# Kernel tuning notes

Hardware: AMD Instinct MI355X
Metric: run time of the kernel (lower is better)

The kernel has to match this reference:

```python
import jax, jax.numpy as jnp
import numpy as np

KERNEL_MUL = 2.0
KERNEL_NUM = 5


def setup_inputs() -> dict:
    key = jax.random.key(0)
    k1, k2 = jax.random.split(key)
    source = jax.random.normal(k1, (4096, 256), dtype=jnp.float32)
    target = jax.random.normal(k2, (4096, 256), dtype=jnp.float32)
    return {"source": source, "target": target}


def reference(source, target):
    n = source.shape[0]
    m = target.shape[0]
    total = jnp.concatenate([source, target], axis=0)  # [n+m, d]
    N = n + m
    # pairwise squared L2 distances via GEMM identity (same math as expand-based)
    sq = jnp.sum(total * total, axis=1)  # [N]
    d2 = sq[:, None] + sq[None, :] - 2.0 * (total @ total.T)  # [N, N]
    d2 = jnp.maximum(d2, 0.0)
    # bandwidth from detached distances (torch uses L2_distance.data)
    bandwidth = jax.lax.stop_gradient(jnp.sum(d2)) / (N * N - N)
    bandwidth = bandwidth / (KERNEL_MUL ** (KERNEL_NUM // 2))
    kernels = jnp.zeros_like(d2)
    for i in range(KERNEL_NUM):  # fixed small loop over bandwidths
        kernels = kernels + jnp.exp(-d2 / (bandwidth * (KERNEL_MUL ** i)))
    XX = jnp.mean(kernels[:n, :n])
    YY = jnp.mean(kernels[n:, n:])
    XY = jnp.mean(kernels[:n, n:])
    YX = jnp.mean(kernels[n:, :n])
    return XX + YY - XY - YX
```

## Files before the change

kernel.cpp:

```cpp
#include <hip/hip_runtime.h>
#include <hip/hip_bf16.h>
#include <stdint.h>
#include <math.h>

#define D     256
#define NTOT  8192
#define NSRC  4096
#define NT    64
#define NTRI  (NT * (NT + 1) / 2)
#define PREPB 256

using f32x4 = __attribute__((ext_vector_type(4))) float;

#define GLB_AS __attribute__((address_space(1)))
#define LDS_AS __attribute__((address_space(3)))

#if __has_builtin(__builtin_amdgcn_exp2f)
#define EXP2F __builtin_amdgcn_exp2f
#else
#define EXP2F exp2f
#endif

__device__ inline unsigned char f32_to_e4m3(float v) {
  uint32_t u = __float_as_uint(v);
  uint32_t s = (u >> 24) & 0x80u;
  uint32_t m = u & 0x7FFFFFFFu;
  if (m <= 0x3C000000u) return (unsigned char)s;
  if (m <  0x3C800000u) return (unsigned char)(s | 0x08u);
  if (m >= 0x43F00000u) return (unsigned char)(s | 0x7Eu);
  uint32_t r = m + 0x0007FFFFu + ((m >> 20) & 1u);
  uint32_t e = (r >> 23) - 127u + 7u;
  return (unsigned char)(s | (e << 3) | ((r >> 20) & 7u));
}
__device__ inline float e4m3_to_f32(unsigned char q) {
  uint32_t s = ((uint32_t)(q & 0x80u)) << 24;
  uint32_t em = q & 0x7Fu;
  if (em == 0) return __uint_as_float(s);
  uint32_t e = (em >> 3) + 120u;
  return __uint_as_float(s | (e << 23) | ((em & 7u) << 20));
}

#define OFF_XB   ((size_t)0)
#define OFF_SQ   ((size_t)NTOT * D)
#define OFF_CP   (OFF_SQ + (size_t)NTOT * 4)
#define OFF_SP   (OFF_CP + (size_t)PREPB * 256 * 4)
#define OFF_CF   (OFF_SP + (size_t)PREPB * 4)
#define OFF_PT   (OFF_CF + 32)
#define OFF_END  (OFF_PT + (size_t)NTRI * 4)

__global__ __launch_bounds__(256) void prep_kernel(
    const float* __restrict__ src, const float* __restrict__ tgt,
    unsigned char* __restrict__ xb, float* __restrict__ sq,
    float* __restrict__ colpart, float* __restrict__ sqpart)
{
  __shared__ float scol4[4][256];
  __shared__ float sSl[4];
  const int tid = threadIdx.x, wave = tid >> 6, lane = tid & 63;
  const int row0 = blockIdx.x * 32 + wave * 8;
  const float* p0 = (row0 < NSRC) ? (src + (size_t)row0 * D)
                                  : (tgt + (size_t)(row0 - NSRC) * D);
  float c0 = 0.f, c1 = 0.f, c2 = 0.f, c3 = 0.f, swave = 0.f;
  for (int rr = 0; rr < 8; ++rr) {
    const int row = row0 + rr;
    const float4 v = reinterpret_cast<const float4*>(p0 + (size_t)rr * D)[lane];
    uchar4 h;
    h.x = f32_to_e4m3(v.x); h.y = f32_to_e4m3(v.y);
    h.z = f32_to_e4m3(v.z); h.w = f32_to_e4m3(v.w);
    reinterpret_cast<uchar4*>(xb + (size_t)row * D)[lane] = h;
    const float f0 = e4m3_to_f32(h.x), f1 = e4m3_to_f32(h.y),
                f2 = e4m3_to_f32(h.z), f3 = e4m3_to_f32(h.w);
    c0 += f0; c1 += f1; c2 += f2; c3 += f3;
    float s = f0 * f0 + f1 * f1 + f2 * f2 + f3 * f3;
    #pragma unroll
    for (int off = 32; off > 0; off >>= 1) s += __shfl_down(s, off);
    if (lane == 0) { sq[row] = s; swave += s; }
  }
  scol4[wave][lane * 4 + 0] = c0;
  scol4[wave][lane * 4 + 1] = c1;
  scol4[wave][lane * 4 + 2] = c2;
  scol4[wave][lane * 4 + 3] = c3;
  if (lane == 0) sSl[wave] = swave;
  __syncthreads();
  colpart[blockIdx.x * 256 + tid] =
      scol4[0][tid] + scol4[1][tid] + scol4[2][tid] + scol4[3][tid];
  if (tid == 0) sqpart[blockIdx.x] = sSl[0] + sSl[1] + sSl[2] + sSl[3];
}

__global__ __launch_bounds__(256) void bw_kernel(
    const float* __restrict__ colpart, const float* __restrict__ sqpart,
    float* __restrict__ cf)
{
  __shared__ float red[256];
  const int t = threadIdx.x;
  float cs = 0.f;
  for (int b = 0; b < PREPB; ++b) cs += colpart[b * 256 + t];
  red[t] = cs * cs;
  __syncthreads();
  for (int off = 128; off > 0; off >>= 1) {
    if (t < off) red[t] += red[t + off];
    __syncthreads();
  }
  const float s2 = red[0];
  __syncthreads();
  red[t] = (t < PREPB) ? sqpart[t] : 0.f;
  __syncthreads();
  for (int off = 128; off > 0; off >>= 1) {
    if (t < off) red[t] += red[t + off];
    __syncthreads();
  }
  if (t == 0) {
    const double sumd2 = 2.0 * (double)NTOT * (double)red[0] - 2.0 * (double)s2;
    const double bw = sumd2 / ((double)NTOT * (double)NTOT - (double)NTOT) / 4.0;
    cf[0] = (float)(-1.4426950408889634 / (bw * 16.0));
  }
}

__global__ __launch_bounds__(256) void pair_kernel(
    const unsigned char* __restrict__ xb, const float* __restrict__ sq,
    const float* __restrict__ cf, float* __restrict__ part)
{
  const int idx = (blockIdx.x & 7) * (NTRI / 8) + (blockIdx.x >> 3);
  const float rr = sqrtf(4160.25f - 2.0f * (float)idx);
  int bi = (int)(64.5f - rr);
  while (NT * (bi + 1) - (bi + 1) * bi / 2 <= idx) ++bi;
  while (NT * bi - bi * (bi - 1) / 2 > idx) --bi;
  const int bj = bi + (idx - (NT * bi - bi * (bi - 1) / 2));

  __shared__ __align__(16) unsigned char lA[128 * 128];
  __shared__ __align__(16) unsigned char lB[128 * 128];
  __shared__ float sqA[128], sqB[128], wsum[4];

  const int tid = threadIdx.x, wave = tid >> 6, lane = tid & 63;
  const int wr = wave >> 1, wc = wave & 1;

  const float c4 = cf[0];
  if (tid < 128) sqA[tid] = sq[bi * 128 + tid];
  else           sqB[tid - 128] = sq[bj * 128 + (tid - 128)];

  const unsigned char* gA0 =
      xb + (size_t)(bi * 128 + wave * 32 + (lane >> 3)) * D + ((lane & 7) ^ (lane >> 3)) * 16;
  const unsigned char* gB0 =
      xb + (size_t)(bj * 128 + wave * 32 + (lane >> 3)) * D + ((lane & 7) ^ (lane >> 3)) * 16;
  char* dA = (char*)lA + wave * 4096;
  char* dB = (char*)lB + wave * 4096;

#define STAGE(t) do {                                                        \
    _Pragma("unroll")                                                        \
    for (int q = 0; q < 4; ++q) {                                            \
      __builtin_amdgcn_global_load_lds(                                      \
          (const GLB_AS uint32_t*)(gA0 + (size_t)q * 8 * D + (t) * 128),     \
          (LDS_AS uint32_t*)(dA + q * 1024), 16, 0, 0);                      \
      __builtin_amdgcn_global_load_lds(                                      \
          (const GLB_AS uint32_t*)(gB0 + (size_t)q * 8 * D + (t) * 128),     \
          (LDS_AS uint32_t*)(dB + q * 1024), 16, 0, 0);                      \
    } } while (0)

  f32x4 acc[4][4];
  #pragma unroll
  for (int mi = 0; mi < 4; ++mi)
    #pragma unroll
    for (int nj = 0; nj < 4; ++nj)
      acc[mi][nj] = (f32x4){0.f, 0.f, 0.f, 0.f};

  const int g = lane >> 4, r7 = lane & 7, rlow = lane & 15;
  const int off8 = (g & 1) * 8, ghalf = g >> 1;

  #pragma unroll
  for (int t = 0; t < 2; ++t) {
    STAGE(t);
    __syncthreads();
    #pragma unroll
    for (int ks = 0; ks < 4; ++ks) {
      const int slot = (2 * ks + ghalf);
      long af[4], bf[4];
      #pragma unroll
      for (int mi = 0; mi < 4; ++mi) {
        const int rowA = wr * 64 + mi * 16 + rlow;
        af[mi] = *(const long*)((const char*)lA + rowA * 128 +
                                (((slot ^ r7)) << 4) + off8);
      }
      #pragma unroll
      for (int nj = 0; nj < 4; ++nj) {
        const int rowB = wc * 64 + nj * 16 + rlow;
        bf[nj] = *(const long*)((const char*)lB + rowB * 128 +
                                (((slot ^ r7)) << 4) + off8);
      }
      #pragma unroll
      for (int mi = 0; mi < 4; ++mi)
        #pragma unroll
        for (int nj = 0; nj < 4; ++nj)
          acc[mi][nj] = __builtin_amdgcn_mfma_f32_16x16x32_fp8_fp8(
              af[mi], bf[nj], acc[mi][nj], 0, 0, 0);
    }
    if (t == 0) __syncthreads();
  }
#undef STAGE

  const int r0c = (lane >> 4) * 4, cc = lane & 15;
  float sjv[4];
  #pragma unroll
  for (int nj = 0; nj < 4; ++nj) sjv[nj] = sqB[wc * 64 + nj * 16 + cc];
  float tsum = 0.f;
  #pragma unroll
  for (int mi = 0; mi < 4; ++mi) {
    #pragma unroll
    for (int r = 0; r < 4; ++r) {
      const float si = sqA[wr * 64 + mi * 16 + r0c + r];
      #pragma unroll
      for (int nj = 0; nj < 4; ++nj) {
        float d2 = fmaf(-2.f, acc[mi][nj][r], si + sjv[nj]);
        d2 = fmaxf(d2, 0.f);
        const float e4 = EXP2F(d2 * c4);
        const float e3 = e4 * e4, e2 = e3 * e3;
        const float e1 = e2 * e2, e0 = e1 * e1;
        tsum += ((e4 + e3) + (e2 + e1)) + e0;
      }
    }
  }
  #pragma unroll
  for (int off = 32; off > 0; off >>= 1) tsum += __shfl_down(tsum, off);
  if (lane == 0) wsum[wave] = tsum;
  __syncthreads();
  if (tid == 0) part[idx] = wsum[0] + wsum[1] + wsum[2] + wsum[3];
}

__global__ __launch_bounds__(256) void out_kernel(
    const float* __restrict__ part, float* __restrict__ out)
{
  __shared__ double red0[256], red1[256], red2[256];
  const int t = threadIdx.x;
  double a0 = 0.0, a1 = 0.0, a2 = 0.0;
  for (int j = t; j < NTRI; j += 256) {
    const float r1 = sqrtf(4160.25f - 2.0f * (float)j);
    int bi = (int)(64.5f - r1);
    while (NT * (bi + 1) - (bi + 1) * bi / 2 <= j) ++bi;
    while (NT * bi - bi * (bi - 1) / 2 > j) --bi;
    const int bj = bi + (j - (NT * bi - bi * (bi - 1) / 2));
    const double w = (bi == bj) ? 1.0 : 2.0;
    const double v = w * (double)part[j];
    if (bi >= 32) a1 += v;
    else if (bj >= 32) a2 += v;
    else a0 += v;
  }
  red0[t] = a0; red1[t] = a1; red2[t] = a2;
  __syncthreads();
  for (int off = 128; off > 0; off >>= 1) {
    if (t < off) {
      red0[t] += red0[t + off];
      red1[t] += red1[t + off];
      red2[t] += red2[t + off];
    }
    __syncthreads();
  }
  if (t == 0)
    out[0] = (float)((red0[0] + red1[0] - red2[0]) /
                     ((double)NSRC * (double)NSRC));
}

extern "C" void kernel_launch(void* const* d_in, const int* in_sizes, int n_in,
                              void* d_out, int out_size, void* d_ws, size_t ws_size,
                              hipStream_t stream) {
  (void)in_sizes; (void)n_in; (void)out_size; (void)ws_size;
  const float* src = (const float*)d_in[0];
  const float* tgt = (const float*)d_in[1];
  char* ws = (char*)d_ws;
  unsigned char* xb = (unsigned char*)(ws + OFF_XB);
  float* sq      = (float*)(ws + OFF_SQ);
  float* colpart = (float*)(ws + OFF_CP);
  float* sqpart  = (float*)(ws + OFF_SP);
  float* cf      = (float*)(ws + OFF_CF);
  float* part    = (float*)(ws + OFF_PT);

  prep_kernel<<<PREPB, 256, 0, stream>>>(src, tgt, xb, sq, colpart, sqpart);
  bw_kernel<<<1, 256, 0, stream>>>(colpart, sqpart, cf);
  pair_kernel<<<NTRI, 256, 0, stream>>>(xb, sq, cf, part);
  out_kernel<<<1, 256, 0, stream>>>(part, (float*)d_out);
}
```

Before: 52.35 us.

## Double-buffer fp8 K-tiles in LDS with async prefetch and widen final reduction

Splits the K dimension of the pair kernel into four 64-byte chunks held in two ping-pong LDS buffers. The next chunk is prefetched with global_load_lds while MFMAs run on the current one, using explicit vmcnt waits, raw s_barrier calls and setprio around the MFMA block. The aim is to hide global-load latency that the old stage-then-sync loop exposed. The final reduction kernel also moves from 256 to 1024 threads. The cost is more barriers per tile and a new XOR swizzle for the narrower rows that must stay correct.

```diff
diff --git a/kernel.cpp b/kernel.cpp
--- a/kernel.cpp
+++ b/kernel.cpp
@@ -126,8 +126,8 @@
   while (NT * bi - bi * (bi - 1) / 2 > idx) --bi;
   const int bj = bi + (idx - (NT * bi - bi * (bi - 1) / 2));
 
-  __shared__ __align__(16) unsigned char lA[128 * 128];
-  __shared__ __align__(16) unsigned char lB[128 * 128];
+  __shared__ __align__(16) unsigned char lA[2][128 * 64];
+  __shared__ __align__(16) unsigned char lB[2][128 * 64];
   __shared__ float sqA[128], sqB[128], wsum[4];
 
   const int tid = threadIdx.x, wave = tid >> 6, lane = tid & 63;
@@ -138,21 +138,23 @@
   else           sqB[tid - 128] = sq[bj * 128 + (tid - 128)];
 
   const unsigned char* gA0 =
-      xb + (size_t)(bi * 128 + wave * 32 + (lane >> 3)) * D + ((lane & 7) ^ (lane >> 3)) * 16;
+      xb + (size_t)(bi * 128 + wave * 32 + (lane >> 2)) * D
+         + (((lane & 3) ^ ((lane >> 2) & 3)) * 16);
   const unsigned char* gB0 =
-      xb + (size_t)(bj * 128 + wave * 32 + (lane >> 3)) * D + ((lane & 7) ^ (lane >> 3)) * 16;
-  char* dA = (char*)lA + wave * 4096;
-  char* dB = (char*)lB + wave * 4096;
-
-#define STAGE(t) do {                                                        \
+      xb + (size_t)(bj * 128 + wave * 32 + (lane >> 2)) * D
+         + (((lane & 3) ^ ((lane >> 2) & 3)) * 16);
+
+#define STAGE(buf, t) do {                                                   \
+    char* dA_ = (char*)lA[buf] + wave * 2048;                                \
+    char* dB_ = (char*)lB[buf] + wave * 2048;                                \
     _Pragma("unroll")                                                        \
-    for (int q = 0; q < 4; ++q) {                                            \
+    for (int q = 0; q < 2; ++q) {                                            \
       __builtin_amdgcn_global_load_lds(                                      \
-          (const GLB_AS uint32_t*)(gA0 + (size_t)q * 8 * D + (t) * 128),     \
-          (LDS_AS uint32_t*)(dA + q * 1024), 16, 0, 0);                      \
+          (const GLB_AS uint32_t*)(gA0 + (size_t)q * 16 * D + (t) * 64),     \
+          (LDS_AS uint32_t*)(dA_ + q * 1024), 16, 0, 0);                     \
       __builtin_amdgcn_global_load_lds(                                      \
-          (const GLB_AS uint32_t*)(gB0 + (size_t)q * 8 * D + (t) * 128),     \
-          (LDS_AS uint32_t*)(dB + q * 1024), 16, 0, 0);                      \
+          (const GLB_AS uint32_t*)(gB0 + (size_t)q * 16 * D + (t) * 64),     \
+          (LDS_AS uint32_t*)(dB_ + q * 1024), 16, 0, 0);                     \
     } } while (0)
 
   f32x4 acc[4][4];
@@ -162,37 +164,50 @@
     for (int nj = 0; nj < 4; ++nj)
       acc[mi][nj] = (f32x4){0.f, 0.f, 0.f, 0.f};
 
-  const int g = lane >> 4, r7 = lane & 7, rlow = lane & 15;
+  const int g = lane >> 4, rlow = lane & 15, r3 = lane & 3;
   const int off8 = (g & 1) * 8, ghalf = g >> 1;
 
-  #pragma unroll
-  for (int t = 0; t < 2; ++t) {
-    STAGE(t);
-    __syncthreads();
-    #pragma unroll
-    for (int ks = 0; ks < 4; ++ks) {
-      const int slot = (2 * ks + ghalf);
+  STAGE(0, 0);
+  #pragma unroll
+  for (int t = 0; t < 4; ++t) {
+    if (t < 3) STAGE((t + 1) & 1, t + 1);
+    __builtin_amdgcn_sched_barrier(0);
+    if (t == 0)      asm volatile("s_waitcnt vmcnt(4) lgkmcnt(0)" ::: "memory");
+    else if (t < 3)  asm volatile("s_waitcnt vmcnt(4)" ::: "memory");
+    else             asm volatile("s_waitcnt vmcnt(0)" ::: "memory");
+    __builtin_amdgcn_s_barrier();
+    __builtin_amdgcn_sched_barrier(0);
+
+    const char* bufA = (const char*)lA[t & 1];
+    const char* bufB = (const char*)lB[t & 1];
+    #pragma unroll
+    for (int ks = 0; ks < 2; ++ks) {
+      const int sw = (((ks * 2 + ghalf) ^ r3) << 4) + off8;
       long af[4], bf[4];
       #pragma unroll
       for (int mi = 0; mi < 4; ++mi) {
         const int rowA = wr * 64 + mi * 16 + rlow;
-        af[mi] = *(const long*)((const char*)lA + rowA * 128 +
-                                (((slot ^ r7)) << 4) + off8);
+        af[mi] = *(const long*)(bufA + rowA * 64 + sw);
       }
       #pragma unroll
       for (int nj = 0; nj < 4; ++nj) {
         const int rowB = wc * 64 + nj * 16 + rlow;
-        bf[nj] = *(const long*)((const char*)lB + rowB * 128 +
-                                (((slot ^ r7)) << 4) + off8);
+        bf[nj] = *(const long*)(bufB + rowB * 64 + sw);
       }
+      __builtin_amdgcn_s_setprio(1);
       #pragma unroll
       for (int mi = 0; mi < 4; ++mi)
         #pragma unroll
         for (int nj = 0; nj < 4; ++nj)
           acc[mi][nj] = __builtin_amdgcn_mfma_f32_16x16x32_fp8_fp8(
               af[mi], bf[nj], acc[mi][nj], 0, 0, 0);
-    }
-    if (t == 0) __syncthreads();
+      __builtin_amdgcn_s_setprio(0);
+    }
+    if (t < 3) {
+      __builtin_amdgcn_sched_barrier(0);
+      __builtin_amdgcn_s_barrier();
+      __builtin_amdgcn_sched_barrier(0);
+    }
   }
 #undef STAGE
 
@@ -224,13 +239,13 @@
   if (tid == 0) part[idx] = wsum[0] + wsum[1] + wsum[2] + wsum[3];
 }
 
-__global__ __launch_bounds__(256) void out_kernel(
+__global__ __launch_bounds__(1024) void out_kernel(
     const float* __restrict__ part, float* __restrict__ out)
 {
-  __shared__ double red0[256], red1[256], red2[256];
+  __shared__ double red0[1024], red1[1024], red2[1024];
   const int t = threadIdx.x;
   double a0 = 0.0, a1 = 0.0, a2 = 0.0;
-  for (int j = t; j < NTRI; j += 256) {
+  for (int j = t; j < NTRI; j += 1024) {
     const float r1 = sqrtf(4160.25f - 2.0f * (float)j);
     int bi = (int)(64.5f - r1);
     while (NT * (bi + 1) - (bi + 1) * bi / 2 <= j) ++bi;
@@ -244,7 +259,7 @@
   }
   red0[t] = a0; red1[t] = a1; red2[t] = a2;
   __syncthreads();
-  for (int off = 128; off > 0; off >>= 1) {
+  for (int off = 512; off > 0; off >>= 1) {
     if (t < off) {
       red0[t] += red0[t + off];
       red1[t] += red1[t + off];
@@ -274,5 +289,5 @@
   prep_kernel<<<PREPB, 256, 0, stream>>>(src, tgt, xb, sq, colpart, sqpart);
   bw_kernel<<<1, 256, 0, stream>>>(colpart, sqpart, cf);
   pair_kernel<<<NTRI, 256, 0, stream>>>(xb, sq, cf, part);
-  out_kernel<<<1, 256, 0, stream>>>(part, (float*)d_out);
-}
+  out_kernel<<<1, 1024, 0, stream>>>(part, (float*)d_out);
+}
```

Result: slower. 58.90 us (+12.5%).
